# Kernel optimization log

Measured on AMD Instinct MI355X. Metric: run time of the kernel, lower is better.

The kernel has to match this reference:

```python
import jax, jax.numpy as jnp
import numpy as np
import math

MUL = 128
N_NODES = 10000
N_EDGES = 131072
AVG_NEIGH = 16.0
# (l1 of node irrep, l2 of edge SH, output l3); sorted by output irrep like e3nn Irreps.sort
INSTR = [(0, 0, 0), (1, 1, 0), (0, 1, 1), (1, 0, 1), (1, 2, 1), (0, 2, 2), (1, 1, 2), (1, 3, 2), (0, 3, 3), (1, 2, 3)]
SH_OFF = [0, 1, 4, 9]  # offsets of l-blocks inside edge_attrs (dim 16 = 1+3+5+7)


def _su2_cg(j1, j2, j3):
    f = math.factorial
    C = np.zeros((2 * j1 + 1, 2 * j2 + 1, 2 * j3 + 1))
    for m1 in range(-j1, j1 + 1):
        for m2 in range(-j2, j2 + 1):
            m3 = m1 + m2
            if abs(m3) > j3:
                continue
            pref = (2 * j3 + 1) * f(j3 + j1 - j2) * f(j3 - j1 + j2) * f(j1 + j2 - j3) / f(j1 + j2 + j3 + 1)
            pref *= f(j3 + m3) * f(j3 - m3) * f(j1 - m1) * f(j1 + m1) * f(j2 - m2) * f(j2 + m2)
            s = 0.0
            for k in range(max(0, -(j3 - j2 + m1), -(j3 - j1 - m2)), min(j1 + j2 - j3, j1 - m1, j2 + m2) + 1):
                s += (-1.0) ** k / (f(k) * f(j1 + j2 - j3 - k) * f(j1 - m1 - k) * f(j2 + m2 - k) * f(j3 - j2 + m1 + k) * f(j3 - j1 - m2 + k))
            C[m1 + j1, m2 + j2, m3 + j3] = math.sqrt(pref) * s
    return C


def _q(l):
    # change of basis real->complex spherical harmonics (e3nn convention incl. (-i)^l phase)
    q = np.zeros((2 * l + 1, 2 * l + 1), dtype=np.complex128)
    for m in range(-l, 0):
        q[l + m, l + abs(m)] = 1 / math.sqrt(2)
        q[l + m, l - abs(m)] = -1j / math.sqrt(2)
    q[l, l] = 1.0
    for m in range(1, l + 1):
        q[l + m, l + abs(m)] = (-1) ** m / math.sqrt(2)
        q[l + m, l - abs(m)] = 1j * (-1) ** m / math.sqrt(2)
    return ((-1j) ** l) * q


def _w3j(l1, l2, l3):
    C = _su2_cg(l1, l2, l3).astype(np.complex128)
    Q1, Q2, Q3 = _q(l1), _q(l2), _q(l3)
    for q3 in (np.conj(Q3), Q3):
        D = np.einsum('abc,ai,bj,ck->ijk', C, Q1, Q2, q3)
        if np.abs(D.imag).max() < 1e-9:
            Dr = D.real
            return (Dr / np.linalg.norm(Dr)).astype(np.float32)
    raise ValueError('real wigner-3j construction failed')


W3J = {ins: _w3j(ins[0], ins[1], ins[2]) for ins in set(INSTR)}


def setup_inputs():
    ks = jax.random.split(jax.random.key(0), 15)
    return {
        'node_feats': jax.random.normal(ks[0], (N_NODES, 4 * MUL), jnp.float32),
        'node_attrs': jax.random.normal(ks[1], (N_NODES, 10), jnp.float32),
        'edge_attrs': jax.random.normal(ks[2], (N_EDGES, 16), jnp.float32),
        'edge_feats': jax.random.normal(ks[3], (N_EDGES, 8), jnp.float32),
        'edge_index': jax.random.randint(ks[4], (2, N_EDGES), 0, N_NODES, jnp.int32),
        'W_node_0': jax.random.normal(ks[5], (MUL, MUL), jnp.float32),
        'W_node_1': jax.random.normal(ks[6], (MUL, MUL), jnp.float32),
        'R_W0': jax.random.normal(ks[7], (8, 64), jnp.float32),
        'R_W1': jax.random.normal(ks[8], (64, 64), jnp.float32),
        'R_W2': jax.random.normal(ks[9], (64, 64), jnp.float32),
        'R_W3': jax.random.normal(ks[10], (64, len(INSTR) * MUL), jnp.float32),
        'W_out_0': jax.random.normal(ks[11], (2 * MUL, MUL), jnp.float32),
        'W_out_1': jax.random.normal(ks[12], (3 * MUL, MUL), jnp.float32),
        'W_out_2': jax.random.normal(ks[13], (3 * MUL, MUL), jnp.float32),
        'W_out_3': jax.random.normal(ks[14], (2 * MUL, MUL), jnp.float32),
    }


def reference(node_feats, node_attrs, edge_attrs, edge_feats, edge_index, W_node_0, W_node_1, R_W0, R_W1, R_W2, R_W3, W_out_0, W_out_1, W_out_2, W_out_3):
    sender, receiver = edge_index[0], edge_index[1]
    n = node_feats.shape[0]
    # self-interaction Linear (e3nn: per-irrep matmul, weight / sqrt(fan_in))
    h0 = jnp.einsum('nui,uv->nvi', node_feats[:, :MUL].reshape(n, MUL, 1), W_node_0) / math.sqrt(MUL)
    h1 = jnp.einsum('nui,uv->nvi', node_feats[:, MUL:].reshape(n, MUL, 3), W_node_1) / math.sqrt(MUL)
    # radial MLP [8,64,64,64,1280] with SiLU on hidden layers
    r = edge_feats
    for W in (R_W0, R_W1, R_W2):
        r = jax.nn.silu(r @ (W / math.sqrt(W.shape[0])))
    r = r @ (R_W3 / math.sqrt(R_W3.shape[0]))
    hs = (h0[sender], h1[sender])  # gather sender feats, [E, MUL, 2l1+1]
    outs = {0: [], 1: [], 2: [], 3: []}
    for k, (l1, l2, l3) in enumerate(INSTR):
        w3j = jnp.asarray(W3J[(l1, l2, l3)])
        sh = edge_attrs[:, SH_OFF[l2]:SH_OFF[l2] + 2 * l2 + 1]
        w = r[:, k * MUL:(k + 1) * MUL]
        hw = hs[l1] * w[:, :, None]                                    # radial-weighted sender feats
        c = jnp.einsum('ijk,ej->eik', w3j, sh)                         # [E, 2l1+1, 2l3+1]
        t = jnp.einsum('eik,eui->euk', c, hw) * math.sqrt(2 * l3 + 1)  # 'uvu' path, component-norm path weight
        outs[l3].append(jax.ops.segment_sum(t, receiver, num_segments=n))
    Wout = (W_out_0, W_out_1, W_out_2, W_out_3)
    blocks = []
    for l in range(4):
        cat = jnp.concatenate(outs[l], axis=1)  # simplify(): concat multiplicities per l
        blocks.append(jnp.einsum('nui,uv->nvi', cat, Wout[l]) / (math.sqrt(cat.shape[1]) * AVG_NEIGH))
    return jnp.concatenate(blocks, axis=-1)  # reshape_irreps -> [N, MUL, 16]
```

## Files before the change

kernel.cpp:

```cpp
#include <hip/hip_runtime.h>
#include <math.h>

#define NNODES 10000
#define NEDGES 131072
#define CHUNK 16

#define W3J_OFF 0
#define H_OFF   1280
#define R2_OFF  (1280 + NNODES*512)
#define CC_OFF  (R2_OFF + NEDGES*64)
#define CSR_W   (CC_OFF + NEDGES*88)
#define CNT_W   CSR_W
#define CUR_W   (CSR_W + NNODES)
#define OFF_W   (CSR_W + 2*NNODES)
#define ELIST_W (CSR_W + 2*NNODES + NNODES + 1)

constexpr int cL1[10]  = {0,1,0,1,1,0,1,1,0,1};
constexpr int cL2[10]  = {0,1,1,0,2,2,1,3,3,2};
constexpr int cN3[10]  = {1,1,3,3,3,5,5,5,7,7};
constexpr int cSHO[10] = {0,1,1,0,4,4,1,9,9,4};
constexpr int cCCO[11] = {0,1,4,7,16,25,30,45,60,67,88};
constexpr int cCATO[10]= {0,128,256,640,1024,1408,2048,2688,3328,4224};

struct cpx { double re, im; };
__device__ inline cpx cmul(cpx a, cpx b){ return {a.re*b.re - a.im*b.im, a.re*b.im + a.im*b.re}; }

__device__ double dfact(int n){ double r = 1.0; for (int i = 2; i <= n; ++i) r *= (double)i; return r; }

__device__ double cgval(int j1,int j2,int j3,int m1,int m2){
  int m3 = m1 + m2;
  if (m3 > j3 || m3 < -j3) return 0.0;
  double pref = (double)(2*j3+1) * dfact(j3+j1-j2)*dfact(j3-j1+j2)*dfact(j1+j2-j3)/dfact(j1+j2+j3+1);
  pref *= dfact(j3+m3)*dfact(j3-m3)*dfact(j1-m1)*dfact(j1+m1)*dfact(j2-m2)*dfact(j2+m2);
  int k0 = 0; if (-(j3-j2+m1) > k0) k0 = -(j3-j2+m1); if (-(j3-j1-m2) > k0) k0 = -(j3-j1-m2);
  int k1 = j1+j2-j3; if (j1-m1 < k1) k1 = j1-m1; if (j2+m2 < k1) k1 = j2+m2;
  double s = 0.0;
  for (int k = k0; k <= k1; ++k){
    double d = dfact(k)*dfact(j1+j2-j3-k)*dfact(j1-m1-k)*dfact(j2+m2-k)*dfact(j3-j2+m1+k)*dfact(j3-j1-m2+k);
    s += ((k & 1) ? -1.0 : 1.0) / d;
  }
  return sqrt(pref) * s;
}

__device__ cpx qval(int l, int a, int col){
  int m = a - l;
  const double is2 = 0.70710678118654752440;
  double re = 0.0, im = 0.0;
  if (m < 0){
    if (col == l - m) re = is2;
    else if (col == l + m) im = -is2;
  } else if (m == 0){
    if (col == l) re = 1.0;
  } else {
    double sgn = (m & 1) ? -1.0 : 1.0;
    if (col == l + m) re = sgn * is2;
    else if (col == l - m) im = sgn * is2;
  }
  double pr, pi;
  switch (l & 3){ case 0: pr=1; pi=0; break; case 1: pr=0; pi=-1; break; case 2: pr=-1; pi=0; break; default: pr=0; pi=1; }
  return { re*pr - im*pi, re*pi + im*pr };
}

__global__ void w3j_kernel(float* ws){
  __shared__ double red[128];
  __shared__ int useConjS;
  __shared__ double normS;
  const int IL[10][3] = {{0,0,0},{1,1,0},{0,1,1},{1,0,1},{1,2,1},{0,2,2},{1,1,2},{1,3,2},{0,3,3},{1,2,3}};
  int k = blockIdx.x;
  int l1 = IL[k][0], l2 = IL[k][1], l3 = IL[k][2];
  int n1 = 2*l1+1, n2 = 2*l2+1, n3 = 2*l3+1;
  int nent = n1*n2*n3;
  int tid = threadIdx.x;
  double dcr=0, dci=0, dpr=0, dpi=0;
  if (tid < nent){
    int i = tid/(n2*n3), j = (tid/n3)%n2, kk = tid%n3;
    for (int a = 0; a < n1; ++a){
      for (int b = 0; b < n2; ++b){
        int m1 = a - l1, m2 = b - l2, m3 = m1 + m2;
        if (m3 < -l3 || m3 > l3) continue;
        int c = m3 + l3;
        double C = cgval(l1,l2,l3,m1,m2);
        if (C == 0.0) continue;
        cpx q1 = qval(l1,a,i), q2 = qval(l2,b,j), q3 = qval(l3,c,kk);
        cpx t = cmul(q1,q2);
        cpx q3c = { q3.re, -q3.im };
        cpx tc = cmul(t, q3c);
        cpx tp = cmul(t, q3);
        dcr += C*tc.re; dci += C*tc.im;
        dpr += C*tp.re; dpi += C*tp.im;
      }
    }
  }
  red[tid] = (tid < nent) ? fabs(dci) : 0.0;
  __syncthreads();
  if (tid == 0){
    double mx = 0.0;
    for (int t = 0; t < 128; ++t) if (red[t] > mx) mx = red[t];
    useConjS = (mx < 1e-9) ? 1 : 0;
  }
  __syncthreads();
  double re = useConjS ? dcr : dpr;
  red[tid] = (tid < nent) ? re*re : 0.0;
  __syncthreads();
  if (tid == 0){
    double s = 0.0;
    for (int t = 0; t < 128; ++t) s += red[t];
    normS = sqrt(s);
  }
  __syncthreads();
  if (tid < nent)
    ws[W3J_OFF + k*128 + tid] = (float)(re / normS * sqrt((double)(2*l3+1)));
}

__launch_bounds__(256, 4)
__global__ void node_kernel(const float* __restrict__ nf, const float* __restrict__ W0,
                            const float* __restrict__ W1, float* __restrict__ ws){
  __shared__ float AtL[128*68];
  float* h = ws + H_OFF;
  int tid = threadIdx.x;
  int n0 = blockIdx.x * 64;
  const float rs = 0.08838834764831845f;
  int mg = (tid & 15) * 4;
  int vg = (tid >> 4) * 8;
  for (int c = 0; c < 4; ++c){
    __syncthreads();
    for (int idx = tid; idx < 8192; idx += 256){
      int m = idx >> 7, u = idx & 127;
      int node = n0 + m;
      float v = 0.f;
      if (node < NNODES)
        v = (c == 0) ? nf[(size_t)node*512 + u] : nf[(size_t)node*512 + 128 + u*3 + (c-1)];
      AtL[u*68 + m] = v;
    }
    __syncthreads();
    const float* W = (c == 0) ? W0 : W1;
    float acc[8][4];
    #pragma unroll
    for (int a = 0; a < 8; ++a){ acc[a][0]=0.f; acc[a][1]=0.f; acc[a][2]=0.f; acc[a][3]=0.f; }
    for (int u = 0; u < 128; ++u){
      float4 am = *(const float4*)&AtL[u*68 + mg];
      const float* wr = W + u*128 + vg;
      float4 b0 = *(const float4*)wr;
      float4 b1 = *(const float4*)(wr + 4);
      float aa[4] = {am.x, am.y, am.z, am.w};
      float bb[8] = {b0.x,b0.y,b0.z,b0.w,b1.x,b1.y,b1.z,b1.w};
      #pragma unroll
      for (int a = 0; a < 8; ++a)
        #pragma unroll
        for (int e = 0; e < 4; ++e)
          acc[a][e] += bb[a]*aa[e];
    }
    #pragma unroll
    for (int e = 0; e < 4; ++e){
      int node = n0 + mg + e;
      if (node < NNODES){
        float4 s0 = {acc[0][e]*rs, acc[1][e]*rs, acc[2][e]*rs, acc[3][e]*rs};
        float4 s1 = {acc[4][e]*rs, acc[5][e]*rs, acc[6][e]*rs, acc[7][e]*rs};
        *(float4*)&h[(size_t)node*512 + c*128 + vg] = s0;
        *(float4*)&h[(size_t)node*512 + c*128 + vg + 4] = s1;
      }
    }
  }
}

template<int KDIM>
__device__ __forceinline__ void mlp_layer(const float* __restrict__ Wg, const float* aL,
                                          float* oL, int tid, float scale){
  int eg = (tid & 15) * 4;
  int jg = (tid >> 4) * 4;
  float acc[4][4];
  #pragma unroll
  for (int a = 0; a < 4; ++a){ acc[a][0]=0.f; acc[a][1]=0.f; acc[a][2]=0.f; acc[a][3]=0.f; }
  #pragma unroll 4
  for (int i = 0; i < KDIM; ++i){
    float4 a4 = *(const float4*)&aL[i*68 + eg];
    float4 b4 = *(const float4*)&Wg[i*64 + jg];
    float aa[4] = {a4.x,a4.y,a4.z,a4.w};
    float bb[4] = {b4.x,b4.y,b4.z,b4.w};
    #pragma unroll
    for (int a = 0; a < 4; ++a)
      #pragma unroll
      for (int e = 0; e < 4; ++e)
        acc[a][e] += bb[a]*aa[e];
  }
  #pragma unroll
  for (int a = 0; a < 4; ++a){
    float4 st;
    float x0 = acc[a][0]*scale; st.x = x0/(1.f + expf(-x0));
    float x1 = acc[a][1]*scale; st.y = x1/(1.f + expf(-x1));
    float x2 = acc[a][2]*scale; st.z = x2/(1.f + expf(-x2));
    float x3 = acc[a][3]*scale; st.w = x3/(1.f + expf(-x3));
    *(float4*)&oL[(jg+a)*68 + eg] = st;
  }
}

__launch_bounds__(256)
__global__ void r2_kernel(const float* __restrict__ ef,
                          const float* __restrict__ RW0, const float* __restrict__ RW1,
                          const float* __restrict__ RW2, float* __restrict__ wsf){
  __shared__ float bufA[64*68];
  __shared__ float bufB[64*68];
  __shared__ float r2T[64*68];
  float* R2 = wsf + R2_OFF;
  int tid = threadIdx.x;
  int eb = blockIdx.x * 64;
  float* efT = r2T;
  for (int idx = tid; idx < 512; idx += 256){
    int e = idx >> 3, i2 = idx & 7;
    efT[i2*68 + e] = ef[(size_t)(eb+e)*8 + i2];
  }
  __syncthreads();
  mlp_layer<8 >(RW0, efT, bufA, tid, 0.35355339059327373f);
  __syncthreads();
  mlp_layer<64>(RW1, bufA, bufB, tid, 0.125f);
  __syncthreads();
  mlp_layer<64>(RW2, bufB, r2T, tid, 0.125f);
  __syncthreads();
  for (int idx = tid; idx < 4096; idx += 256){
    int e = idx >> 6, i = idx & 63;
    R2[((size_t)(eb+e) << 6) + i] = r2T[i*68 + e];
  }
}

__device__ __forceinline__ float cc_compute(int r, const float* w3L, const float* she){
  float v = 0.f;
  #pragma unroll
  for (int in = 0; in < 10; ++in){
    if (r >= cCCO[in] && r < cCCO[in+1]){
      int rr = r - cCCO[in];
      const int N3v = cN3[in];
      const int N2v = 2*cL2[in] + 1;
      int i = rr / N3v;
      int q = rr - i*N3v;
      float s = 0.f;
      for (int j = 0; j < N2v; ++j)
        s += w3L[in*128 + (i*N2v + j)*N3v + q] * she[cSHO[in] + j];
      v = s;
    }
  }
  return v;
}

__launch_bounds__(256)
__global__ void cc_kernel(const float* __restrict__ ea, float* __restrict__ wsf){
  __shared__ float w3L[1280];
  __shared__ float shE[32*16];
  float* ccG = wsf + CC_OFF;
  int tid = threadIdx.x;
  int eb = blockIdx.x * 32;
  for (int idx = tid; idx < 1280; idx += 256) w3L[idx] = wsf[W3J_OFF + idx];
  for (int idx = tid; idx < 512; idx += 256){
    int e = idx >> 4, j = idx & 15;
    shE[e*16 + j] = ea[((size_t)(eb+e) << 4) + j];
  }
  __syncthreads();
  for (int idx = tid; idx < 32*88; idx += 256){
    int e = idx / 88, r = idx - e*88;
    ccG[(size_t)(eb+e)*88 + r] = cc_compute(r, w3L, shE + e*16);
  }
}

__global__ void hist_kernel(const int* __restrict__ ei, int* __restrict__ cnt){
  int e = blockIdx.x*256 + threadIdx.x;
  if (e < NEDGES) atomicAdd(&cnt[ei[NEDGES + e]], 1);
}

__global__ void scan_kernel(const int* __restrict__ cnt, int* __restrict__ off){
  __shared__ int part[256];
  __shared__ int partp[256];
  int t = threadIdx.x;
  const int S = 40;
  int s = 0;
  for (int j = 0; j < S; ++j){ int idx = t*S + j; if (idx < NNODES) s += cnt[idx]; }
  part[t] = s;
  __syncthreads();
  if (t == 0){ int run = 0; for (int i = 0; i < 256; ++i){ partp[i] = run; run += part[i]; } }
  __syncthreads();
  int run = partp[t];
  for (int j = 0; j < S; ++j){
    int idx = t*S + j;
    if (idx <= NNODES){
      off[idx] = run;
      if (idx < NNODES) run += cnt[idx];
    }
  }
}

__global__ void fill_kernel(const int* __restrict__ ei, const int* __restrict__ off,
                            int* __restrict__ cur, int* __restrict__ elist){
  int e = blockIdx.x*256 + threadIdx.x;
  if (e < NEDGES){
    int r = ei[NEDGES + e];
    int p = off[r] + atomicAdd(&cur[r], 1);
    elist[p] = e;
  }
}

template<int IN>
__device__ __forceinline__ void tp_g(const float* __restrict__ cce, const float* __restrict__ hp,
                                     float wv, float* accm){
  constexpr int N3v = cN3[IN];
  if constexpr (cL1[IN] == 0){
    float wh = wv * hp[0];
    #pragma unroll
    for (int q = 0; q < N3v; ++q) accm[q] += cce[q] * wh;
  } else {
    float wa = wv * hp[128];
    float wb = wv * hp[256];
    float wc = wv * hp[384];
    #pragma unroll
    for (int q = 0; q < N3v; ++q)
      accm[q] += cce[q]*wa + cce[N3v+q]*wb + cce[2*N3v+q]*wc;
  }
}

template<int M>
__device__ __forceinline__ void do_m(const float* __restrict__ RW3, const float* r2L,
                                     const float* ccL, const float* __restrict__ h,
                                     const int* sC, int tid, int u, int i0, float* accm){
  float wv[CHUNK];
  #pragma unroll
  for (int e = 0; e < CHUNK; ++e) wv[e] = 0.f;
  const float* rw = RW3 + 256*M + tid;
  #pragma unroll 4
  for (int i = 0; i < 64; ++i){
    float b = rw[(size_t)i*1280];
    const float* rr = &r2L[i*20];
    float4 r0 = *(const float4*)&rr[0];
    float4 r1 = *(const float4*)&rr[4];
    float4 r2v= *(const float4*)&rr[8];
    float4 r3 = *(const float4*)&rr[12];
    wv[0]  += b*r0.x;  wv[1]  += b*r0.y;  wv[2]  += b*r0.z;  wv[3]  += b*r0.w;
    wv[4]  += b*r1.x;  wv[5]  += b*r1.y;  wv[6]  += b*r1.z;  wv[7]  += b*r1.w;
    wv[8]  += b*r2v.x; wv[9]  += b*r2v.y; wv[10] += b*r2v.z; wv[11] += b*r2v.w;
    wv[12] += b*r3.x;  wv[13] += b*r3.y;  wv[14] += b*r3.z;  wv[15] += b*r3.w;
  }
  #pragma unroll
  for (int e = 0; e < CHUNK; ++e) wv[e] *= 0.125f;
  #pragma unroll
  for (int eh = 0; eh < 2; ++eh){
    if (i0 == 0){
      #pragma unroll
      for (int e8 = 0; e8 < 8; ++e8){
        int e = eh*8 + e8;
        const float* hp = h + ((size_t)sC[e] << 9) + u;
        tp_g<2*M>(ccL + e*88 + cCCO[2*M], hp, wv[e], accm);
      }
    } else {
      #pragma unroll
      for (int e8 = 0; e8 < 8; ++e8){
        int e = eh*8 + e8;
        const float* hp = h + ((size_t)sC[e] << 9) + u;
        tp_g<2*M+1>(ccL + e*88 + cCCO[2*M+1], hp, wv[e], accm);
      }
    }
  }
}

template<int IN>
__device__ __forceinline__ void st_cat(float* catL, int u, const float* accm){
  constexpr int N3v = cN3[IN];
  float* p = catL + cCATO[IN] + u*N3v;
  #pragma unroll
  for (int q = 0; q < N3v; ++q) p[q] = accm[q];
}

template<int L>
__device__ __forceinline__ void out_l(const float* catL, const float* __restrict__ Wo,
                                      float* __restrict__ outp, int n, int v){
  constexpr int NI = 2*L + 1;
  constexpr int UL = (L==0 || L==3) ? 256 : 384;
  constexpr int GOv = (L==0) ? 0 : (L==1) ? 256 : (L==2) ? 1408 : 3328;
  constexpr int OOv = (L==0) ? 0 : (L==1) ? 1 : (L==2) ? 4 : 9;
  const float scale = (L==0 || L==3) ? 0.00390625f : 0.0031894435433133252f;
  float o[NI];
  #pragma unroll
  for (int i = 0; i < NI; ++i) o[i] = 0.f;
  #pragma unroll 4
  for (int ul = 0; ul < UL; ++ul){
    float wv = Wo[(size_t)ul*128 + v];
    const float* a = catL + GOv + ul*NI;
    #pragma unroll
    for (int i = 0; i < NI; ++i) o[i] += a[i]*wv;
  }
  float* op = outp + (size_t)n*2048 + v*16 + OOv;
  #pragma unroll
  for (int i = 0; i < NI; ++i) op[i] = o[i]*scale;
}

__launch_bounds__(256, 7)
__global__ void gather_kernel(const int* __restrict__ ei,
                              const float* __restrict__ RW3,
                              const float* __restrict__ Wo0, const float* __restrict__ Wo1,
                              const float* __restrict__ Wo2, const float* __restrict__ Wo3,
                              const float* __restrict__ wsf,
                              const int* __restrict__ off, const int* __restrict__ elist,
                              float* __restrict__ outp){
  __shared__ float smemF[5120];
  int*   idsL = (int*)smemF;
  int*   idsC = (int*)(smemF + 512);
  int*   sC   = (int*)(smemF + 528);
  float* r2L  = smemF + 544;
  float* ccL  = smemF + 1824;
  float* catL = smemF;

  const float* h   = wsf + H_OFF;
  const float* R2  = wsf + R2_OFF;
  const float* ccG = wsf + CC_OFF;
  int nblk = blockIdx.x, tid = threadIdx.x;
  int beg = off[nblk], end = off[nblk+1];
  int deg = end - beg;
  int degc = deg < 512 ? deg : 512;
  for (int idx = tid; idx < degc; idx += 256) idsL[idx] = elist[beg + idx];
  __syncthreads();
  {
    int v0 = 0, r0 = 0, v1 = 0, r1 = 0;
    bool a0 = tid < degc, a1 = tid + 256 < degc;
    if (a0){ v0 = idsL[tid]; int r = 0; for (int j = 0; j < degc; ++j) r += (idsL[j] < v0); r0 = r; }
    if (a1){ v1 = idsL[tid+256]; int r = 0; for (int j = 0; j < degc; ++j) r += (idsL[j] < v1); r1 = r; }
    __syncthreads();
    if (a0) idsL[r0] = v0;
    if (a1) idsL[r1] = v1;
  }

  int u = tid & 127;
  int i0 = tid >> 7;
  float acc0[1] = {0.f};
  float acc1[3] = {0.f,0.f,0.f};
  float acc2[5] = {0.f,0.f,0.f,0.f,0.f};
  float acc3[5] = {0.f,0.f,0.f,0.f,0.f};
  float acc4[7] = {0.f,0.f,0.f,0.f,0.f,0.f,0.f};

  for (int base = 0; base < deg; base += CHUNK){
    int eN = deg - base; if (eN > CHUNK) eN = CHUNK;
    __syncthreads();
    if (tid < CHUNK){
      int k = base + tid;
      int id;
      if (tid < eN) id = (k < degc) ? idsL[k] : elist[beg + k];
      else          id = (base < degc) ? idsL[base] : elist[beg + base];
      idsC[tid] = id;
      sC[tid]   = ei[id];
    }
    __syncthreads();
    for (int idx = tid; idx < (CHUNK << 6); idx += 256){
      int e = idx >> 6, i = idx & 63;
      r2L[i*20 + e] = (e < eN) ? R2[((size_t)idsC[e] << 6) + i] : 0.f;
    }
    for (int idx = tid; idx < CHUNK*88; idx += 256){
      int e = idx / 88, r = idx - e*88;
      ccL[idx] = ccG[(size_t)idsC[e]*88 + r];
    }
    __syncthreads();
    do_m<0>(RW3, r2L, ccL, h, sC, tid, u, i0, acc0);
    do_m<1>(RW3, r2L, ccL, h, sC, tid, u, i0, acc1);
    do_m<2>(RW3, r2L, ccL, h, sC, tid, u, i0, acc2);
    do_m<3>(RW3, r2L, ccL, h, sC, tid, u, i0, acc3);
    do_m<4>(RW3, r2L, ccL, h, sC, tid, u, i0, acc4);
  }
  __syncthreads();
  if (i0 == 0){
    st_cat<0>(catL, u, acc0);
    st_cat<2>(catL, u, acc1);
    st_cat<4>(catL, u, acc2);
    st_cat<6>(catL, u, acc3);
    st_cat<8>(catL, u, acc4);
  } else {
    st_cat<1>(catL, u, acc0);
    st_cat<3>(catL, u, acc1);
    st_cat<5>(catL, u, acc2);
    st_cat<7>(catL, u, acc3);
    st_cat<9>(catL, u, acc4);
  }
  __syncthreads();
  if (i0 == 0){
    out_l<0>(catL, Wo0, outp, nblk, u);
    out_l<2>(catL, Wo2, outp, nblk, u);
  } else {
    out_l<1>(catL, Wo1, outp, nblk, u);
    out_l<3>(catL, Wo3, outp, nblk, u);
  }
}

extern "C" void kernel_launch(void* const* d_in, const int* in_sizes, int n_in,
                              void* d_out, int out_size, void* d_ws, size_t ws_size,
                              hipStream_t stream){
  const float* nf  = (const float*)d_in[0];
  const float* ea  = (const float*)d_in[2];
  const float* ef  = (const float*)d_in[3];
  const int*   ei  = (const int*)d_in[4];
  const float* W0  = (const float*)d_in[5];
  const float* W1  = (const float*)d_in[6];
  const float* RW0 = (const float*)d_in[7];
  const float* RW1 = (const float*)d_in[8];
  const float* RW2 = (const float*)d_in[9];
  const float* RW3 = (const float*)d_in[10];
  const float* Wo0 = (const float*)d_in[11];
  const float* Wo1 = (const float*)d_in[12];
  const float* Wo2 = (const float*)d_in[13];
  const float* Wo3 = (const float*)d_in[14];
  float* wsf  = (float*)d_ws;
  int*   wsi  = (int*)d_ws;
  float* outp = (float*)d_out;

  hipMemsetAsync(wsi + CNT_W, 0, 2*NNODES*sizeof(int), stream);
  w3j_kernel<<<10, 128, 0, stream>>>(wsf);
  node_kernel<<<157, 256, 0, stream>>>(nf, W0, W1, wsf);
  r2_kernel<<<2048, 256, 0, stream>>>(ef, RW0, RW1, RW2, wsf);
  cc_kernel<<<4096, 256, 0, stream>>>(ea, wsf);
  hist_kernel<<<512, 256, 0, stream>>>(ei, wsi + CNT_W);
  scan_kernel<<<1, 256, 0, stream>>>(wsi + CNT_W, wsi + OFF_W);
  fill_kernel<<<512, 256, 0, stream>>>(ei, wsi + OFF_W, wsi + CUR_W, wsi + ELIST_W);
  gather_kernel<<<NNODES, 256, 0, stream>>>(ei, RW3, Wo0, Wo1, Wo2, Wo3,
                                            wsf, wsi + OFF_W, wsi + ELIST_W, outp);
}
```

Measured before the change: 1.792 ms.

## Hoist sender feature loads into registers and split edge chunk into halves

Sender node features for eight edges are loaded into registers once and reused across all five radial-weight groups, instead of being re-gathered for every group. The sixteen-edge chunk is processed as two halves of eight, which shrinks the per-group weight accumulator array. The radial weight matrix is read twice per chunk, and launch bounds are relaxed to allow more registers per thread at lower occupancy.

```diff
diff --git a/kernel.cpp b/kernel.cpp
--- a/kernel.cpp
+++ b/kernel.cpp
@@ -297,64 +297,69 @@
 }
 
 template<int IN>
-__device__ __forceinline__ void tp_g(const float* __restrict__ cce, const float* __restrict__ hp,
-                                     float wv, float* accm){
+__device__ __forceinline__ void tp_r(const float* __restrict__ cce, const float* hv,
+                                     float wvv, float* accm){
   constexpr int N3v = cN3[IN];
+  const float* c = cce + cCCO[IN];
   if constexpr (cL1[IN] == 0){
-    float wh = wv * hp[0];
+    float wh = wvv * hv[0];
     #pragma unroll
-    for (int q = 0; q < N3v; ++q) accm[q] += cce[q] * wh;
+    for (int q = 0; q < N3v; ++q) accm[q] += c[q]*wh;
   } else {
-    float wa = wv * hp[128];
-    float wb = wv * hp[256];
-    float wc = wv * hp[384];
+    float wa = wvv*hv[1], wb = wvv*hv[2], wc = wvv*hv[3];
     #pragma unroll
     for (int q = 0; q < N3v; ++q)
-      accm[q] += cce[q]*wa + cce[N3v+q]*wb + cce[2*N3v+q]*wc;
-  }
-}
-
-template<int M>
-__device__ __forceinline__ void do_m(const float* __restrict__ RW3, const float* r2L,
-                                     const float* ccL, const float* __restrict__ h,
-                                     const int* sC, int tid, int u, int i0, float* accm){
-  float wv[CHUNK];
-  #pragma unroll
-  for (int e = 0; e < CHUNK; ++e) wv[e] = 0.f;
+      accm[q] += c[q]*wa + c[N3v+q]*wb + c[2*N3v+q]*wc;
+  }
+}
+
+template<int M, int EOFF>
+__device__ __forceinline__ void do_m8(const float* __restrict__ RW3, const float* r2L,
+                                      const float* ccL, const float hv[][4],
+                                      int tid, int i0, float* accm){
+  float wv[8];
+  #pragma unroll
+  for (int e = 0; e < 8; ++e) wv[e] = 0.f;
   const float* rw = RW3 + 256*M + tid;
   #pragma unroll 4
   for (int i = 0; i < 64; ++i){
     float b = rw[(size_t)i*1280];
-    const float* rr = &r2L[i*20];
+    const float* rr = &r2L[i*20 + EOFF];
     float4 r0 = *(const float4*)&rr[0];
     float4 r1 = *(const float4*)&rr[4];
-    float4 r2v= *(const float4*)&rr[8];
-    float4 r3 = *(const float4*)&rr[12];
-    wv[0]  += b*r0.x;  wv[1]  += b*r0.y;  wv[2]  += b*r0.z;  wv[3]  += b*r0.w;
-    wv[4]  += b*r1.x;  wv[5]  += b*r1.y;  wv[6]  += b*r1.z;  wv[7]  += b*r1.w;
-    wv[8]  += b*r2v.x; wv[9]  += b*r2v.y; wv[10] += b*r2v.z; wv[11] += b*r2v.w;
-    wv[12] += b*r3.x;  wv[13] += b*r3.y;  wv[14] += b*r3.z;  wv[15] += b*r3.w;
-  }
-  #pragma unroll
-  for (int e = 0; e < CHUNK; ++e) wv[e] *= 0.125f;
-  #pragma unroll
-  for (int eh = 0; eh < 2; ++eh){
-    if (i0 == 0){
-      #pragma unroll
-      for (int e8 = 0; e8 < 8; ++e8){
-        int e = eh*8 + e8;
-        const float* hp = h + ((size_t)sC[e] << 9) + u;
-        tp_g<2*M>(ccL + e*88 + cCCO[2*M], hp, wv[e], accm);
-      }
-    } else {
-      #pragma unroll
-      for (int e8 = 0; e8 < 8; ++e8){
-        int e = eh*8 + e8;
-        const float* hp = h + ((size_t)sC[e] << 9) + u;
-        tp_g<2*M+1>(ccL + e*88 + cCCO[2*M+1], hp, wv[e], accm);
-      }
-    }
-  }
+    wv[0] += b*r0.x; wv[1] += b*r0.y; wv[2] += b*r0.z; wv[3] += b*r0.w;
+    wv[4] += b*r1.x; wv[5] += b*r1.y; wv[6] += b*r1.z; wv[7] += b*r1.w;
+  }
+  #pragma unroll
+  for (int e = 0; e < 8; ++e) wv[e] *= 0.125f;
+  #pragma unroll
+  for (int e = 0; e < 8; ++e){
+    const float* cce = ccL + (EOFF + e)*88;
+    if (i0 == 0) tp_r<2*M  >(cce, hv[e], wv[e], accm);
+    else         tp_r<2*M+1>(cce, hv[e], wv[e], accm);
+  }
+}
+
+template<int EOFF>
+__device__ __forceinline__ void do_half(const float* __restrict__ RW3, const float* r2L,
+                                        const float* ccL, const float* __restrict__ h,
+                                        const int* sC, int tid, int u, int i0,
+                                        float* acc0, float* acc1, float* acc2,
+                                        float* acc3, float* acc4){
+  float hv[8][4];
+  #pragma unroll
+  for (int e = 0; e < 8; ++e){
+    const float* hp = h + ((size_t)sC[EOFF + e] << 9) + u;
+    hv[e][0] = hp[0];
+    hv[e][1] = hp[128];
+    hv[e][2] = hp[256];
+    hv[e][3] = hp[384];
+  }
+  do_m8<0,EOFF>(RW3, r2L, ccL, hv, tid, i0, acc0);
+  do_m8<1,EOFF>(RW3, r2L, ccL, hv, tid, i0, acc1);
+  do_m8<2,EOFF>(RW3, r2L, ccL, hv, tid, i0, acc2);
+  do_m8<3,EOFF>(RW3, r2L, ccL, hv, tid, i0, acc3);
+  do_m8<4,EOFF>(RW3, r2L, ccL, hv, tid, i0, acc4);
 }
 
 template<int IN>
@@ -388,7 +393,7 @@
   for (int i = 0; i < NI; ++i) op[i] = o[i]*scale;
 }
 
-__launch_bounds__(256, 7)
+__launch_bounds__(256, 4)
 __global__ void gather_kernel(const int* __restrict__ ei,
                               const float* __restrict__ RW3,
                               const float* __restrict__ Wo0, const float* __restrict__ Wo1,
@@ -452,11 +457,8 @@
       ccL[idx] = ccG[(size_t)idsC[e]*88 + r];
     }
     __syncthreads();
-    do_m<0>(RW3, r2L, ccL, h, sC, tid, u, i0, acc0);
-    do_m<1>(RW3, r2L, ccL, h, sC, tid, u, i0, acc1);
-    do_m<2>(RW3, r2L, ccL, h, sC, tid, u, i0, acc2);
-    do_m<3>(RW3, r2L, ccL, h, sC, tid, u, i0, acc3);
-    do_m<4>(RW3, r2L, ccL, h, sC, tid, u, i0, acc4);
+    do_half<0>(RW3, r2L, ccL, h, sC, tid, u, i0, acc0, acc1, acc2, acc3, acc4);
+    do_half<8>(RW3, r2L, ccL, h, sC, tid, u, i0, acc0, acc1, acc2, acc3, acc4);
   }
   __syncthreads();
   if (i0 == 0){
```

Result: slower. 3.597 ms (+100.8%).
